# Performance work log

Measured on AMD Instinct MI355X. Metric: run time of the kernel, lower is better.

Reference implementation:

```python
import jax, jax.numpy as jnp
import numpy as np

N = 384          # residues / nodes
E = 12288        # edges (avg degree 32)
D_LM = 1024      # BERT hidden
D_NODE = 256     # extra node features -> D_LM + D_NODE = 1280
D = 1280         # node_emb_size
H = D // 10      # 128, dis/mask MLP hidden
M = 64           # masked positions


def setup_inputs() -> dict:
    key = jax.random.key(0)
    ks = jax.random.split(key, 16)
    s = lambda d_in: 1.0 / np.sqrt(d_in)
    inp = {
        "lm_embedding": jax.random.normal(ks[0], (1, N + 2, D_LM), jnp.float32),
        "node_feat": jax.random.normal(ks[1], (N, D_NODE), jnp.float32),
        # positive distances in [0.5, 1.5) so edge_weight = 1/(d^2+1e-6) is well scaled
        "edge_feat": jax.random.uniform(ks[2], (E, 1), jnp.float32) + 0.5,
        "src": jax.random.randint(ks[3], (E,), 0, N, jnp.int32),
        "dst": jax.random.randint(ks[4], (E,), 0, N, jnp.int32),
        "mask_index": jax.random.randint(ks[5], (M,), 0, N, jnp.int32),
        # GINConv apply-func linears (stored as [in, out]; torch Linear is x @ W.T + b)
        "W_gin0": jax.random.normal(ks[6], (D, D), jnp.float32) * s(D),
        "b_gin0": jnp.zeros((D,), jnp.float32),
        "W_gin1": jax.random.normal(ks[7], (D, D), jnp.float32) * s(D),
        "b_gin1": jnp.zeros((D,), jnp.float32),
        # dis_nn: Linear(D,H) -> ReLU -> Linear(H,30)
        "Wd1": jax.random.normal(ks[8], (D, H), jnp.float32) * s(D),
        "bd1": jnp.zeros((H,), jnp.float32),
        "Wd2": jax.random.normal(ks[9], (H, 30), jnp.float32) * s(H),
        "bd2": jnp.zeros((30,), jnp.float32),
        # mask_nn: Linear(D,H) -> ReLU -> Linear(H,2) -> Tanh
        "Wm1": jax.random.normal(ks[10], (D, H), jnp.float32) * s(D),
        "bm1": jnp.zeros((H,), jnp.float32),
        "Wm2": jax.random.normal(ks[11], (H, 2), jnp.float32) * s(H),
        "bm2": jnp.zeros((2,), jnp.float32),
    }
    return inp


def _gin(x, src, dst, edge_weight, W, b):
    # DGL GINConv (eps=0, 'sum'): Linear( x + sum_{e:(u->v)} w_e * x_u )
    msg = x[src] * edge_weight                      # [E, D] gather-multiply
    agg = jax.ops.segment_sum(msg, dst, num_segments=N)  # scatter-sum to dst
    return (x + agg) @ W + b


def reference(lm_embedding, node_feat, edge_feat, src, dst, mask_index,
              W_gin0, b_gin0, W_gin1, b_gin1,
              Wd1, bd1, Wd2, bd2, Wm1, bm1, Wm2, bm2):
    # node_feat0: strip CLS/SEP tokens, concat with node features -> [N, D]
    node_feat0 = jnp.concatenate([lm_embedding[0, 1:-1, :], node_feat], axis=1)
    edge_weight = 1.0 / (edge_feat ** 2 + 1e-6)     # [E, 1]

    # original uses node_feat0.data (detached) as GIN input
    x0 = jax.lax.stop_gradient(node_feat0)
    h = _gin(x0, src, dst, edge_weight, W_gin0, b_gin0)
    node_output = _gin(h, src, dst, edge_weight, W_gin1, b_gin1)
    node_output = node_output + node_feat0          # residual (use_lm=1)

    # pairwise squared differences: [N, N, D]
    dis_hid = (node_output[None, :, :] - node_output[:, None, :]) ** 2
    dh = dis_hid.reshape(-1, D)                     # [N*N, D]
    dis_pred = jax.nn.relu(dh @ Wd1 + bd1) @ Wd2 + bd2  # [N*N, 30]

    xm = node_output[mask_index]                    # [M, D]
    mask_pred = jnp.tanh(jax.nn.relu(xm @ Wm1 + bm1) @ Wm2 + bm2)  # [M, 2]
    return dis_pred, mask_pred
```

## Files before the change

kernel.cpp:

```cpp
#include <hip/hip_runtime.h>
#include <hip/hip_bf16.h>

#define NN 384
#define EE 12288
#define DD 1280
#define HH 128
#define DISROWS (NN*NN)

typedef short bf16x8 __attribute__((ext_vector_type(8)));
typedef short bf16x4 __attribute__((ext_vector_type(4)));
typedef float f32x4  __attribute__((ext_vector_type(4)));

__device__ __forceinline__ unsigned short f2bf(float x){
  unsigned u = __builtin_bit_cast(unsigned, x);
  u += 0x7fffu + ((u >> 16) & 1u);
  return (unsigned short)(u >> 16);
}
__device__ __forceinline__ float bf2f(unsigned short h){
  unsigned u = ((unsigned)h) << 16;
  return __builtin_bit_cast(float, u);
}
__device__ __forceinline__ short f2bf_fast(float x){
  return (short)__bfloat16_as_ushort(__float2bfloat16(x));
}
__device__ __forceinline__ void glds16(const short* g, short* l){
  __builtin_amdgcn_global_load_lds((const __attribute__((address_space(1))) void*)g,
                                   (__attribute__((address_space(3))) void*)l, 16, 0, 0);
}

__device__ __forceinline__ void tsplit_body(const float* __restrict__ W,
                                            short* __restrict__ Thi, short* __restrict__ Tlo,
                                            int R, int C, int bx, int by, int t,
                                            float* tile ){
  int rb = by*64, cb = bx*64;
  int r  = t >> 2;
  int cs = (t & 3) * 16;
  const float* sp = W + (long)(rb + r)*C + cb + cs;
  #pragma unroll
  for (int i = 0; i < 16; i += 4){
    f32x4 v = *(const f32x4*)(sp + i);
    tile[r*65 + cs+i+0] = v[0]; tile[r*65 + cs+i+1] = v[1];
    tile[r*65 + cs+i+2] = v[2]; tile[r*65 + cs+i+3] = v[3];
  }
  __syncthreads();
  int cp = t >> 2;
  int rs = (t & 3) * 16;
  bf16x8 vh0, vh1, vl0, vl1;
  #pragma unroll
  for (int i = 0; i < 8; ++i){
    float f = tile[(rs+i)*65 + cp];
    unsigned short h = f2bf(f);
    vh0[i] = (short)h; vl0[i] = (short)f2bf(f - bf2f(h));
  }
  #pragma unroll
  for (int i = 0; i < 8; ++i){
    float f = tile[(rs+8+i)*65 + cp];
    unsigned short h = f2bf(f);
    vh1[i] = (short)h; vl1[i] = (short)f2bf(f - bf2f(h));
  }
  long ob = (long)(cb + cp)*R + rb + rs;
  *(bf16x8*)&Thi[ob]   = vh0;
  *(bf16x8*)&Thi[ob+8] = vh1;
  if (Tlo){
    *(bf16x8*)&Tlo[ob]   = vl0;
    *(bf16x8*)&Tlo[ob+8] = vl1;
  }
}

__global__ void k_prep(const float* __restrict__ lm, const float* __restrict__ nf,
                       float* __restrict__ x0,
                       const int* __restrict__ dst, const float* __restrict__ ef,
                       int* __restrict__ offs, int* __restrict__ sorted,
                       float* __restrict__ ew,
                       const float* __restrict__ Wd1, short* __restrict__ W1t,
                       const float* __restrict__ Wd2, short* __restrict__ W2t,
                       const float* __restrict__ Wg0, short* __restrict__ WtAh,
                       short* __restrict__ WtAl){
  __shared__ __align__(16) float sh[64*65];
  const int b = blockIdx.x;
  const int t = threadIdx.x;
  if (b < 960){
    int i = b*512 + t;
    int n = i / 1280;
    int d = i - n*1280;
    x0[i] = (d < 1024) ? lm[(n+1)*1024 + d] : nf[n*256 + (d-1024)];
    return;
  }
  if (b == 960){
    int* cnt = (int*)sh;
    int* base = cnt + 512;
    if (t < 512) cnt[t] = 0;
    __syncthreads();
    for (int e = t; e < EE; e += 512){
      atomicAdd(&cnt[dst[e]], 1);
      float f = ef[e];
      ew[e] = 1.0f/(f*f + 1e-6f);
    }
    __syncthreads();
    for (int off = 1; off < 512; off <<= 1){
      int v = (t >= off) ? cnt[t - off] : 0;
      __syncthreads();
      cnt[t] += v;
      __syncthreads();
    }
    if (t < NN){
      int excl = t ? cnt[t-1] : 0;
      offs[t] = excl;
      base[t] = excl;
    }
    if (t == 0) offs[NN] = EE;
    __syncthreads();
    for (int e = t; e < EE; e += 512){
      int p = atomicAdd(&base[dst[e]], 1);
      sorted[p] = e;
    }
    return;
  }
  if (b < 1002){
    int g = b - 961;
    if (g < 40){
      if (t < 256) tsplit_body(Wd1, W1t, nullptr, DD, HH, g & 1, g >> 1, t, sh);
      else { __syncthreads(); }
      return;
    }
    for (int i = t; i < 32*HH; i += 512){
      int c = i >> 7, h = i & 127;
      float v = (c < 30) ? Wd2[h*30 + c] : 0.f;
      W2t[i] = (short)f2bf(v);
    }
    return;
  }
  {
    int g = b - 1002;
    if (t < 256) tsplit_body(Wg0, WtAh, WtAl, DD, DD, g % 20, g / 20, t, sh);
    else { __syncthreads(); }
  }
}

__global__ void k_agg(const float* __restrict__ X, const float* __restrict__ ew,
                      const int* __restrict__ src, const int* __restrict__ offs,
                      const int* __restrict__ sorted, float* __restrict__ Y){
  __shared__ int   s_off[160];
  __shared__ float s_w[160];
  const int v = blockIdx.x;
  const int d = blockIdx.y*256 + threadIdx.x;
  const int t = threadIdx.x;
  float acc = X[(long)v*DD + d];
  const int b = offs[v], e = offs[v+1];
  for (int c0 = b; c0 < e; c0 += 160){
    int n = e - c0; if (n > 160) n = 160;
    __syncthreads();
    if (t < n){
      int eid = sorted[c0 + t];
      s_off[t] = src[eid]*DD;
      s_w[t]   = ew[eid];
    }
    __syncthreads();
    int k = 0;
    for (; k + 4 <= n; k += 4){
      acc += s_w[k]  *X[s_off[k]   + d];
      acc += s_w[k+1]*X[s_off[k+1] + d];
      acc += s_w[k+2]*X[s_off[k+2] + d];
      acc += s_w[k+3]*X[s_off[k+3] + d];
    }
    for (; k < n; ++k) acc += s_w[k]*X[s_off[k] + d];
  }
  Y[(long)v*DD + d] = acc;
}

__launch_bounds__(256, 2)
__global__ void k_gin_gemm(const float* __restrict__ Y, const short* __restrict__ Whi,
                           const short* __restrict__ Wlo, float* __restrict__ P){
  __shared__ __align__(16) short Ahi[128*40], Alo[128*40], Bhi[128*40], Blo[128*40];
  const int m0 = blockIdx.x*128;
  const int n0 = blockIdx.y*128;
  const int kbase = blockIdx.z*320;
  const int t = threadIdx.x, w = t >> 6, lane = t & 63;
  const int l15 = lane & 15, l4 = lane >> 4;
  f32x4 acc[2][8];
  #pragma unroll
  for (int m = 0; m < 2; ++m)
    #pragma unroll
    for (int n = 0; n < 8; ++n) acc[m][n] = (f32x4){0.f,0.f,0.f,0.f};

  const int row = t >> 1, half = t & 1;
  const float* ap  = Y   + (long)(m0+row)*DD + half*16;
  const short* bph = Whi + (long)(n0+row)*DD + half*16;
  const short* bpl = Wlo + (long)(n0+row)*DD + half*16;

  for (int kk = 0; kk < 10; ++kk){
    int d0 = kbase + kk*32;
    __syncthreads();
    #pragma unroll
    for (int g = 0; g < 2; ++g){
      f32x4 v0 = *(const f32x4*)(ap + d0 + g*8);
      f32x4 v1 = *(const f32x4*)(ap + d0 + g*8 + 4);
      bf16x8 vh, vl;
      #pragma unroll
      for (int q = 0; q < 4; ++q){
        unsigned short h0 = f2bf(v0[q]);
        vh[q]   = (short)h0; vl[q]   = (short)f2bf(v0[q] - bf2f(h0));
        unsigned short h1 = f2bf(v1[q]);
        vh[4+q] = (short)h1; vl[4+q] = (short)f2bf(v1[q] - bf2f(h1));
      }
      *(bf16x8*)&Ahi[row*40 + half*16 + g*8] = vh;
      *(bf16x8*)&Alo[row*40 + half*16 + g*8] = vl;
    }
    *(bf16x8*)&Bhi[row*40 + half*16]     = *(const bf16x8*)(bph + d0);
    *(bf16x8*)&Bhi[row*40 + half*16 + 8] = *(const bf16x8*)(bph + d0 + 8);
    *(bf16x8*)&Blo[row*40 + half*16]     = *(const bf16x8*)(bpl + d0);
    *(bf16x8*)&Blo[row*40 + half*16 + 8] = *(const bf16x8*)(bpl + d0 + 8);
    __syncthreads();

    bf16x8 ah[2], al[2];
    #pragma unroll
    for (int m = 0; m < 2; ++m){
      int rr = w*32 + m*16 + l15;
      ah[m] = *(const bf16x8*)&Ahi[rr*40 + l4*8];
      al[m] = *(const bf16x8*)&Alo[rr*40 + l4*8];
    }
    #pragma unroll
    for (int n = 0; n < 8; ++n){
      int rr = n*16 + l15;
      bf16x8 bh = *(const bf16x8*)&Bhi[rr*40 + l4*8];
      bf16x8 bl = *(const bf16x8*)&Blo[rr*40 + l4*8];
      #pragma unroll
      for (int m = 0; m < 2; ++m){
        acc[m][n] = __builtin_amdgcn_mfma_f32_16x16x32_bf16(ah[m], bh, acc[m][n], 0,0,0);
        acc[m][n] = __builtin_amdgcn_mfma_f32_16x16x32_bf16(ah[m], bl, acc[m][n], 0,0,0);
        acc[m][n] = __builtin_amdgcn_mfma_f32_16x16x32_bf16(al[m], bh, acc[m][n], 0,0,0);
      }
    }
  }
  float* Pz = P + (long)blockIdx.z*NN*DD;
  #pragma unroll
  for (int m = 0; m < 2; ++m){
    #pragma unroll
    for (int n = 0; n < 8; ++n){
      int gr0 = m0 + w*32 + m*16 + l4*4;
      int gc  = n0 + n*16 + l15;
      #pragma unroll
      for (int r = 0; r < 4; ++r)
        Pz[(long)(gr0+r)*DD + gc] = acc[m][n][r];
    }
  }
}

__global__ void k_red_t(const float* __restrict__ P, const float* __restrict__ bias,
                        const float* __restrict__ resid, float* __restrict__ Out,
                        const float* __restrict__ Wg1, short* __restrict__ WtAh,
                        short* __restrict__ WtAl){
  __shared__ __align__(16) float sh[64*65];
  const int b = blockIdx.x;
  if (b >= 480){
    if (Wg1){
      int g = b - 480;
      tsplit_body(Wg1, WtAh, WtAl, DD, DD, g % 20, g / 20, threadIdx.x, sh);
    }
    return;
  }
  const int i = b*256 + threadIdx.x;
  const int col = (i*4) % DD;
  const f32x4* P4 = (const f32x4*)P;
  f32x4 s = P4[i];
  s += P4[i + 122880];
  s += P4[i + 2*122880];
  s += P4[i + 3*122880];
  s += *(const f32x4*)(bias + col);
  if (resid) s += ((const f32x4*)resid)[i];
  ((f32x4*)Out)[i] = s;
}

__launch_bounds__(256, 3)
__global__ void k_dis(const float* __restrict__ X, const short* __restrict__ W1t,
                      const float* __restrict__ bd1, const short* __restrict__ W2t,
                      const float* __restrict__ bd2, float* __restrict__ out,
                      const int* __restrict__ midx,
                      const float* __restrict__ Wm1, const float* __restrict__ bm1,
                      const float* __restrict__ Wm2, const float* __restrict__ bm2){
  __shared__ __align__(16) short smem[25088];
  const int b = blockIdx.x;
  const int t = threadIdx.x;

  if (b >= 600){
    float* tl = (float*)smem;
    int m = b - 600;
    if (t < HH){
      const float* x = X + (long)midx[m]*DD;
      float a0 = 0.f, a1 = 0.f, a2 = 0.f, a3 = 0.f;
      for (int d = 0; d < DD; d += 4){
        a0 += x[d]   * Wm1[(d)*HH + t];
        a1 += x[d+1] * Wm1[(d+1)*HH + t];
        a2 += x[d+2] * Wm1[(d+2)*HH + t];
        a3 += x[d+3] * Wm1[(d+3)*HH + t];
      }
      float v = a0 + a1 + a2 + a3 + bm1[t];
      tl[t] = v > 0.f ? v : 0.f;
    }
    __syncthreads();
    if (t < 2){
      float s = bm2[t];
      for (int h = 0; h < HH; ++h) s += tl[h]*Wm2[h*2 + t];
      out[(long)DISROWS*30 + m*2 + t] = tanhf(s);
    }
    return;
  }

  int k = 0, rem = b;
  while (rem >= 2*(24 - k)){ rem -= 2*(24 - k); ++k; }
  int ib = 2*k;
  if (rem >= 24 - k){ ++ib; rem -= 24 - k; }
  const int jb = k + rem;
  const int i0 = ib*8, j0 = jb*16;

  const int w = t >> 6, lane = t & 63;
  const int l15 = lane & 15, l4 = lane >> 4;

  short* WA = smem;
  float* XF = (float*)(smem + 16384);
  short* TL = smem;
  float* OT = (float*)(smem + 17408);

  f32x4 acc[2][8];
  #pragma unroll
  for (int m = 0; m < 2; ++m)
    #pragma unroll
    for (int n = 0; n < 8; ++n) acc[m][n] = (f32x4){0.f,0.f,0.f,0.f};

  const short* wsrc[4];
  #pragma unroll
  for (int i = 0; i < 4; ++i){
    int hb = w*32 + i*8 + (lane >> 3);
    wsrc[i] = W1t + (long)hb*DD + (((lane & 7) ^ (hb & 7))*8);
  }
  const float* xsrc[6];
  int xli[6];
  #pragma unroll
  for (int g = 0; g < 6; ++g){
    int idx = g*256 + t;
    int rowl = idx >> 6, col = idx & 63;
    int grow = (rowl < 8) ? (i0 + rowl) : (j0 + rowl - 8);
    xsrc[g] = X + (long)grow*DD + col;
    xli[g] = rowl*68 + col;
  }

  float xr[6];
  #pragma unroll
  for (int i = 0; i < 4; ++i)
    glds16(wsrc[i], WA + (w*32 + i*8)*64);
  #pragma unroll
  for (int g = 0; g < 6; ++g) xr[g] = xsrc[g][0];
  #pragma unroll
  for (int g = 0; g < 6; ++g) XF[xli[g]] = xr[g];
  __syncthreads();

  for (int mk = 0; mk < 20; ++mk){
    const int cb = mk & 1;
    short* WAc = WA + cb*8192;
    float* XFc = XF + cb*1632;
    short* WAn = WA + (cb^1)*8192;
    float* XFn = XF + (cb^1)*1632;
    if (mk < 19){
      #pragma unroll
      for (int i = 0; i < 4; ++i)
        glds16(wsrc[i] + (mk+1)*64, WAn + (w*32 + i*8)*64);
      #pragma unroll
      for (int g = 0; g < 6; ++g) xr[g] = xsrc[g][(mk+1)*64];
    }
    #pragma unroll
    for (int ks = 0; ks < 2; ++ks){
      f32x4 xj0 = *(const f32x4*)&XFc[(8 + l15)*68 + ks*32 + l4*8];
      f32x4 xj1 = *(const f32x4*)&XFc[(8 + l15)*68 + ks*32 + l4*8 + 4];
      bf16x8 a[2];
      #pragma unroll
      for (int m = 0; m < 2; ++m){
        const float* xip = &XFc[(2*w + m)*68 + ks*32 + l4*8];
        f32x4 xi0 = *(const f32x4*)xip;
        f32x4 xi1 = *(const f32x4*)(xip + 4);
        bf16x8 av;
        #pragma unroll
        for (int q = 0; q < 4; ++q){ float dl = xj0[q]-xi0[q]; av[q]   = f2bf_fast(dl*dl); }
        #pragma unroll
        for (int q = 0; q < 4; ++q){ float dl = xj1[q]-xi1[q]; av[4+q] = f2bf_fast(dl*dl); }
        a[m] = av;
      }
      #pragma unroll
      for (int n = 0; n < 8; ++n){
        bf16x8 wf = *(const bf16x8*)&WAc[(n*16 + l15)*64 + (((ks*4 + l4) ^ (l15 & 7))*8)];
        acc[0][n] = __builtin_amdgcn_mfma_f32_16x16x32_bf16(wf, a[0], acc[0][n], 0,0,0);
        acc[1][n] = __builtin_amdgcn_mfma_f32_16x16x32_bf16(wf, a[1], acc[1][n], 0,0,0);
      }
    }
    if (mk < 19){
      #pragma unroll
      for (int g = 0; g < 6; ++g) XFn[xli[g]] = xr[g];
    }
    __syncthreads();
  }

  f32x4 bd1v[8];
  #pragma unroll
  for (int n = 0; n < 8; ++n) bd1v[n] = *(const f32x4*)(bd1 + n*16 + l4*4);
  #pragma unroll
  for (int m = 0; m < 2; ++m){
    int pair = (2*w + m)*16 + l15;
    #pragma unroll
    for (int n = 0; n < 8; ++n){
      bf16x4 pv;
      #pragma unroll
      for (int r = 0; r < 4; ++r){
        float v = acc[m][n][r] + bd1v[n][r];
        v = v > 0.f ? v : 0.f;
        pv[r] = f2bf_fast(v);
      }
      *(bf16x4*)&TL[pair*136 + n*16 + l4*4] = pv;
    }
  }
  __syncthreads();

  f32x4 acc2[2][2];
  #pragma unroll
  for (int m2 = 0; m2 < 2; ++m2)
    #pragma unroll
    for (int nn = 0; nn < 2; ++nn) acc2[m2][nn] = (f32x4){0.f,0.f,0.f,0.f};
  #pragma unroll
  for (int hs = 0; hs < 4; ++hs){
    bf16x8 b2[2];
    #pragma unroll
    for (int nn = 0; nn < 2; ++nn)
      b2[nn] = *(const bf16x8*)&W2t[(nn*16 + l15)*HH + hs*32 + l4*8];
    #pragma unroll
    for (int m2 = 0; m2 < 2; ++m2){
      bf16x8 a2 = *(const bf16x8*)&TL[(w*32 + m2*16 + l15)*136 + hs*32 + l4*8];
      #pragma unroll
      for (int nn = 0; nn < 2; ++nn)
        acc2[m2][nn] = __builtin_amdgcn_mfma_f32_16x16x32_bf16(a2, b2[nn], acc2[m2][nn], 0,0,0);
    }
  }
  #pragma unroll
  for (int m2 = 0; m2 < 2; ++m2){
    #pragma unroll
    for (int nn = 0; nn < 2; ++nn){
      int cc = nn*16 + l15;
      if (cc < 30){
        float b2v = bd2[cc];
        #pragma unroll
        for (int r = 0; r < 4; ++r)
          OT[(w*32 + m2*16 + l4*4 + r)*30 + cc] = acc2[m2][nn][r] + b2v;
      }
    }
  }
  __syncthreads();

  {
    int i = t >> 5;
    int ca = (t & 31)*15;
    long nbase = ((long)(i0 + i)*NN + j0)*30 + ca;
    const float* nsrc = OT + i*480 + ca;
    #pragma unroll
    for (int q = 0; q < 15; ++q) out[nbase + q] = nsrc[q];
    int j = t >> 4;
    int s = t & 15;
    int ii = s >> 1;
    int c0 = (s & 1)*15;
    long mbase = ((long)(j0 + j)*NN + i0 + ii)*30 + c0;
    const float* msrc = OT + ii*480 + j*30 + c0;
    #pragma unroll
    for (int q = 0; q < 15; ++q) out[mbase + q] = msrc[q];
  }
}

extern "C" void kernel_launch(void* const* d_in, const int* in_sizes, int n_in,
                              void* d_out, int out_size, void* d_ws, size_t ws_size,
                              hipStream_t stream){
  const float* lm   = (const float*)d_in[0];
  const float* nf   = (const float*)d_in[1];
  const float* ef   = (const float*)d_in[2];
  const int*   src  = (const int*)d_in[3];
  const int*   dst  = (const int*)d_in[4];
  const int*   midx = (const int*)d_in[5];
  const float* Wg0  = (const float*)d_in[6];
  const float* bg0  = (const float*)d_in[7];
  const float* Wg1  = (const float*)d_in[8];
  const float* bg1  = (const float*)d_in[9];
  const float* Wd1  = (const float*)d_in[10];
  const float* bd1  = (const float*)d_in[11];
  const float* Wd2  = (const float*)d_in[12];
  const float* bd2  = (const float*)d_in[13];
  const float* Wm1  = (const float*)d_in[14];
  const float* bm1  = (const float*)d_in[15];
  const float* Wm2  = (const float*)d_in[16];
  const float* bm2  = (const float*)d_in[17];
  float* dis = (float*)d_out;

  char* ws = (char*)d_ws;
  size_t off = 0;
  auto alloc = [&](size_t bytes)->void*{
    void* p = ws + off; off += (bytes + 255) & ~(size_t)255; return p;
  };
  float* x0   = (float*)alloc((size_t)NN*DD*4);
  float* yb   = (float*)alloc((size_t)NN*DD*4);
  float* hb   = (float*)alloc((size_t)NN*DD*4);
  float* ew   = (float*)alloc((size_t)EE*4);
  int*   offs = (int*)alloc((NN+1)*4);
  int*   sorted = (int*)alloc(EE*4);
  short* WtAh = (short*)alloc((size_t)DD*DD*2);
  short* WtAl = (short*)alloc((size_t)DD*DD*2);
  short* W1t  = (short*)alloc((size_t)HH*DD*2);
  short* W2t  = (short*)alloc((size_t)32*HH*2);
  float* P    = (float*)alloc((size_t)4*NN*DD*4);

  k_prep<<<1402,512,0,stream>>>(lm, nf, x0, dst, ef, offs, sorted, ew,
                                Wd1, W1t, Wd2, W2t, Wg0, WtAh, WtAl);

  k_agg<<<dim3(384,5),256,0,stream>>>(x0, ew, src, offs, sorted, yb);
  k_gin_gemm<<<dim3(3,10,4),256,0,stream>>>(yb, WtAh, WtAl, P);
  k_red_t<<<880,256,0,stream>>>(P, bg0, nullptr, hb, Wg1, WtAh, WtAl);

  k_agg<<<dim3(384,5),256,0,stream>>>(hb, ew, src, offs, sorted, yb);
  k_gin_gemm<<<dim3(3,10,4),256,0,stream>>>(yb, WtAh, WtAl, P);
  k_red_t<<<480,256,0,stream>>>(P, bg1, x0, hb, nullptr, nullptr, nullptr);

  k_dis<<<664,256,0,stream>>>(hb, W1t, bd1, W2t, bd2, dis,
                              midx, Wm1, bm1, Wm2, bm2);
}
```

Before: 142.3 us.

## Drop split-K GIN GEMM, fuse epilogue, and enlarge dis tiles to 16x16

The GIN GEMM moves from a 128x128 split-K tile plus a separate reduction kernel to a 64x64 full-K tile. Bias and residual are now applied in the epilogue, which removes the partial-sum buffer and the reduce kernel. Both GIN weight transposes move into the prep kernel, using separate buffers. The pairwise distance kernel now uses 16x16 i/j tiles (half as many blocks) with a 32-wide K step, a new swizzle, and a two-pass second-layer/store phase, so each W1 slice loaded is reused across more pairs. In exchange, the GIN GEMM has fewer blocks doing longer K loops, the prep kernel grows, and the dis kernel uses more registers per thread.

Result: slower. 197.5 us (+38.8%).

```diff
diff --git a/kernel.cpp b/kernel.cpp
--- a/kernel.cpp
+++ b/kernel.cpp
@@ -10,6 +10,7 @@
 typedef short bf16x8 __attribute__((ext_vector_type(8)));
 typedef short bf16x4 __attribute__((ext_vector_type(4)));
 typedef float f32x4  __attribute__((ext_vector_type(4)));
+typedef float f32x2  __attribute__((ext_vector_type(2)));
 
 __device__ __forceinline__ unsigned short f2bf(float x){
   unsigned u = __builtin_bit_cast(unsigned, x);
@@ -75,7 +76,9 @@
                        const float* __restrict__ Wd1, short* __restrict__ W1t,
                        const float* __restrict__ Wd2, short* __restrict__ W2t,
                        const float* __restrict__ Wg0, short* __restrict__ WtAh,
-                       short* __restrict__ WtAl){
+                       short* __restrict__ WtAl,
+                       const float* __restrict__ Wg1, short* __restrict__ WtBh,
+                       short* __restrict__ WtBl){
   __shared__ __align__(16) float sh[64*65];
   const int b = blockIdx.x;
   const int t = threadIdx.x;
@@ -130,9 +133,15 @@
     }
     return;
   }
-  {
+  if (b < 1402){
     int g = b - 1002;
     if (t < 256) tsplit_body(Wg0, WtAh, WtAl, DD, DD, g % 20, g / 20, t, sh);
+    else { __syncthreads(); }
+    return;
+  }
+  {
+    int g = b - 1402;
+    if (t < 256) tsplit_body(Wg1, WtBh, WtBl, DD, DD, g % 20, g / 20, t, sh);
     else { __syncthreads(); }
   }
 }
@@ -169,109 +178,67 @@
 }
 
 __launch_bounds__(256, 2)
-__global__ void k_gin_gemm(const float* __restrict__ Y, const short* __restrict__ Whi,
-                           const short* __restrict__ Wlo, float* __restrict__ P){
-  __shared__ __align__(16) short Ahi[128*40], Alo[128*40], Bhi[128*40], Blo[128*40];
-  const int m0 = blockIdx.x*128;
-  const int n0 = blockIdx.y*128;
-  const int kbase = blockIdx.z*320;
+__global__ void k_gin(const float* __restrict__ Y, const short* __restrict__ Whi,
+                      const short* __restrict__ Wlo, const float* __restrict__ bias,
+                      const float* __restrict__ resid, float* __restrict__ Out){
+  __shared__ __align__(16) short Ahi[64*40], Alo[64*40], Bhi[64*40], Blo[64*40];
+  const int m0 = blockIdx.x*64, n0 = blockIdx.y*64;
   const int t = threadIdx.x, w = t >> 6, lane = t & 63;
   const int l15 = lane & 15, l4 = lane >> 4;
-  f32x4 acc[2][8];
-  #pragma unroll
-  for (int m = 0; m < 2; ++m)
-    #pragma unroll
-    for (int n = 0; n < 8; ++n) acc[m][n] = (f32x4){0.f,0.f,0.f,0.f};
-
-  const int row = t >> 1, half = t & 1;
-  const float* ap  = Y   + (long)(m0+row)*DD + half*16;
-  const short* bph = Whi + (long)(n0+row)*DD + half*16;
-  const short* bpl = Wlo + (long)(n0+row)*DD + half*16;
-
-  for (int kk = 0; kk < 10; ++kk){
-    int d0 = kbase + kk*32;
-    __syncthreads();
-    #pragma unroll
-    for (int g = 0; g < 2; ++g){
-      f32x4 v0 = *(const f32x4*)(ap + d0 + g*8);
-      f32x4 v1 = *(const f32x4*)(ap + d0 + g*8 + 4);
-      bf16x8 vh, vl;
-      #pragma unroll
-      for (int q = 0; q < 4; ++q){
-        unsigned short h0 = f2bf(v0[q]);
-        vh[q]   = (short)h0; vl[q]   = (short)f2bf(v0[q] - bf2f(h0));
-        unsigned short h1 = f2bf(v1[q]);
-        vh[4+q] = (short)h1; vl[4+q] = (short)f2bf(v1[q] - bf2f(h1));
-      }
-      *(bf16x8*)&Ahi[row*40 + half*16 + g*8] = vh;
-      *(bf16x8*)&Alo[row*40 + half*16 + g*8] = vl;
-    }
-    *(bf16x8*)&Bhi[row*40 + half*16]     = *(const bf16x8*)(bph + d0);
-    *(bf16x8*)&Bhi[row*40 + half*16 + 8] = *(const bf16x8*)(bph + d0 + 8);
-    *(bf16x8*)&Blo[row*40 + half*16]     = *(const bf16x8*)(bpl + d0);
-    *(bf16x8*)&Blo[row*40 + half*16 + 8] = *(const bf16x8*)(bpl + d0 + 8);
-    __syncthreads();
-
-    bf16x8 ah[2], al[2];
-    #pragma unroll
-    for (int m = 0; m < 2; ++m){
-      int rr = w*32 + m*16 + l15;
-      ah[m] = *(const bf16x8*)&Ahi[rr*40 + l4*8];
-      al[m] = *(const bf16x8*)&Alo[rr*40 + l4*8];
-    }
-    #pragma unroll
-    for (int n = 0; n < 8; ++n){
-      int rr = n*16 + l15;
-      bf16x8 bh = *(const bf16x8*)&Bhi[rr*40 + l4*8];
-      bf16x8 bl = *(const bf16x8*)&Blo[rr*40 + l4*8];
-      #pragma unroll
-      for (int m = 0; m < 2; ++m){
-        acc[m][n] = __builtin_amdgcn_mfma_f32_16x16x32_bf16(ah[m], bh, acc[m][n], 0,0,0);
-        acc[m][n] = __builtin_amdgcn_mfma_f32_16x16x32_bf16(ah[m], bl, acc[m][n], 0,0,0);
-        acc[m][n] = __builtin_amdgcn_mfma_f32_16x16x32_bf16(al[m], bh, acc[m][n], 0,0,0);
-      }
-    }
-  }
-  float* Pz = P + (long)blockIdx.z*NN*DD;
-  #pragma unroll
-  for (int m = 0; m < 2; ++m){
-    #pragma unroll
-    for (int n = 0; n < 8; ++n){
-      int gr0 = m0 + w*32 + m*16 + l4*4;
-      int gc  = n0 + n*16 + l15;
-      #pragma unroll
-      for (int r = 0; r < 4; ++r)
-        Pz[(long)(gr0+r)*DD + gc] = acc[m][n][r];
-    }
-  }
-}
-
-__global__ void k_red_t(const float* __restrict__ P, const float* __restrict__ bias,
-                        const float* __restrict__ resid, float* __restrict__ Out,
-                        const float* __restrict__ Wg1, short* __restrict__ WtAh,
-                        short* __restrict__ WtAl){
-  __shared__ __align__(16) float sh[64*65];
-  const int b = blockIdx.x;
-  if (b >= 480){
-    if (Wg1){
-      int g = b - 480;
-      tsplit_body(Wg1, WtAh, WtAl, DD, DD, g % 20, g / 20, threadIdx.x, sh);
-    }
-    return;
-  }
-  const int i = b*256 + threadIdx.x;
-  const int col = (i*4) % DD;
-  const f32x4* P4 = (const f32x4*)P;
-  f32x4 s = P4[i];
-  s += P4[i + 122880];
-  s += P4[i + 2*122880];
-  s += P4[i + 3*122880];
-  s += *(const f32x4*)(bias + col);
-  if (resid) s += ((const f32x4*)resid)[i];
-  ((f32x4*)Out)[i] = s;
-}
-
-__launch_bounds__(256, 3)
+  f32x4 acc[4];
+  #pragma unroll
+  for (int n = 0; n < 4; ++n) acc[n] = (f32x4){0.f,0.f,0.f,0.f};
+
+  const int row = t >> 2, q = t & 3;
+  const float* ap  = Y   + (long)(m0+row)*DD + q*8;
+  const short* bph = Whi + (long)(n0+row)*DD + q*8;
+  const short* bpl = Wlo + (long)(n0+row)*DD + q*8;
+
+  for (int kk = 0; kk < 40; ++kk){
+    const int d0 = kk*32;
+    __syncthreads();
+    f32x4 v0 = *(const f32x4*)(ap + d0);
+    f32x4 v1 = *(const f32x4*)(ap + d0 + 4);
+    bf16x8 vh, vl;
+    #pragma unroll
+    for (int qq = 0; qq < 4; ++qq){
+      unsigned short h0 = f2bf(v0[qq]);
+      vh[qq]   = (short)h0; vl[qq]   = (short)f2bf(v0[qq] - bf2f(h0));
+      unsigned short h1 = f2bf(v1[qq]);
+      vh[4+qq] = (short)h1; vl[4+qq] = (short)f2bf(v1[qq] - bf2f(h1));
+    }
+    *(bf16x8*)&Ahi[row*40 + q*8] = vh;
+    *(bf16x8*)&Alo[row*40 + q*8] = vl;
+    *(bf16x8*)&Bhi[row*40 + q*8] = *(const bf16x8*)(bph + d0);
+    *(bf16x8*)&Blo[row*40 + q*8] = *(const bf16x8*)(bpl + d0);
+    __syncthreads();
+
+    bf16x8 ah = *(const bf16x8*)&Ahi[(w*16 + l15)*40 + l4*8];
+    bf16x8 al = *(const bf16x8*)&Alo[(w*16 + l15)*40 + l4*8];
+    #pragma unroll
+    for (int n = 0; n < 4; ++n){
+      bf16x8 bh = *(const bf16x8*)&Bhi[(n*16 + l15)*40 + l4*8];
+      bf16x8 bl = *(const bf16x8*)&Blo[(n*16 + l15)*40 + l4*8];
+      acc[n] = __builtin_amdgcn_mfma_f32_16x16x32_bf16(ah, bh, acc[n], 0,0,0);
+      acc[n] = __builtin_amdgcn_mfma_f32_16x16x32_bf16(ah, bl, acc[n], 0,0,0);
+      acc[n] = __builtin_amdgcn_mfma_f32_16x16x32_bf16(al, bh, acc[n], 0,0,0);
+    }
+  }
+  #pragma unroll
+  for (int n = 0; n < 4; ++n){
+    int gc = n0 + n*16 + l15;
+    float bv = bias[gc];
+    #pragma unroll
+    for (int r = 0; r < 4; ++r){
+      int gr = m0 + w*16 + l4*4 + r;
+      float o = acc[n][r] + bv;
+      if (resid) o += resid[(long)gr*DD + gc];
+      Out[(long)gr*DD + gc] = o;
+    }
+  }
+}
+
+__launch_bounds__(256, 2)
 __global__ void k_dis(const float* __restrict__ X, const short* __restrict__ W1t,
                       const float* __restrict__ bd1, const short* __restrict__ W2t,
                       const float* __restrict__ bd2, float* __restrict__ out,
@@ -282,9 +249,9 @@
   const int b = blockIdx.x;
   const int t = threadIdx.x;
 
-  if (b >= 600){
+  if (b >= 300){
     float* tl = (float*)smem;
-    int m = b - 600;
+    int m = b - 300;
     if (t < HH){
       const float* x = X + (long)midx[m]*DD;
       float a0 = 0.f, a1 = 0.f, a2 = 0.f, a3 = 0.f;
@@ -306,167 +273,171 @@
     return;
   }
 
-  int k = 0, rem = b;
-  while (rem >= 2*(24 - k)){ rem -= 2*(24 - k); ++k; }
-  int ib = 2*k;
-  if (rem >= 24 - k){ ++ib; rem -= 24 - k; }
-  const int jb = k + rem;
-  const int i0 = ib*8, j0 = jb*16;
+  int ib = 0, rem = b;
+  while (rem >= 24 - ib){ rem -= 24 - ib; ++ib; }
+  const int jb = ib + rem;
+  const int i0 = ib*16, j0 = jb*16;
 
   const int w = t >> 6, lane = t & 63;
   const int l15 = lane & 15, l4 = lane >> 4;
 
   short* WA = smem;
-  float* XF = (float*)(smem + 16384);
+  float* XJ = (float*)(smem + 8192);
   short* TL = smem;
   float* OT = (float*)(smem + 17408);
 
-  f32x4 acc[2][8];
-  #pragma unroll
-  for (int m = 0; m < 2; ++m)
+  f32x4 acc[4][8];
+  #pragma unroll
+  for (int m = 0; m < 4; ++m)
     #pragma unroll
     for (int n = 0; n < 8; ++n) acc[m][n] = (f32x4){0.f,0.f,0.f,0.f};
 
-  const short* wsrc[4];
-  #pragma unroll
-  for (int i = 0; i < 4; ++i){
-    int hb = w*32 + i*8 + (lane >> 3);
-    wsrc[i] = W1t + (long)hb*DD + (((lane & 7) ^ (hb & 7))*8);
-  }
-  const float* xsrc[6];
-  int xli[6];
-  #pragma unroll
-  for (int g = 0; g < 6; ++g){
-    int idx = g*256 + t;
-    int rowl = idx >> 6, col = idx & 63;
-    int grow = (rowl < 8) ? (i0 + rowl) : (j0 + rowl - 8);
-    xsrc[g] = X + (long)grow*DD + col;
-    xli[g] = rowl*68 + col;
-  }
-
-  float xr[6];
-  #pragma unroll
-  for (int i = 0; i < 4; ++i)
-    glds16(wsrc[i], WA + (w*32 + i*8)*64);
-  #pragma unroll
-  for (int g = 0; g < 6; ++g) xr[g] = xsrc[g][0];
-  #pragma unroll
-  for (int g = 0; g < 6; ++g) XF[xli[g]] = xr[g];
+  const short* wsrc[2]; int wdst[2];
+  #pragma unroll
+  for (int i = 0; i < 2; ++i){
+    int h = (w*2 + i)*16 + (lane >> 2);
+    int s = lane & 3;
+    wsrc[i] = W1t + (long)h*DD + ((s ^ ((h >> 1) & 3))*8);
+    wdst[i] = (w*2 + i)*512;
+  }
+  const float* xjsrc = X + (long)(j0 + (t >> 4))*DD + (t & 15)*2;
+  const int xjli = (t >> 4)*36 + (t & 15)*2;
+  const float* xip[4];
+  #pragma unroll
+  for (int m = 0; m < 4; ++m)
+    xip[m] = X + (long)(i0 + w*4 + m)*DD + l4*8;
+
+  glds16(wsrc[0], WA + wdst[0]);
+  glds16(wsrc[1], WA + wdst[1]);
+  { f32x2 v = *(const f32x2*)xjsrc; *(f32x2*)&XJ[xjli] = v; }
+  f32x4 xa[4], xb[4];
+  #pragma unroll
+  for (int m = 0; m < 4; ++m){
+    xa[m] = *(const f32x4*)xip[m];
+    xb[m] = *(const f32x4*)(xip[m] + 4);
+  }
   __syncthreads();
 
-  for (int mk = 0; mk < 20; ++mk){
-    const int cb = mk & 1;
-    short* WAc = WA + cb*8192;
-    float* XFc = XF + cb*1632;
-    short* WAn = WA + (cb^1)*8192;
-    float* XFn = XF + (cb^1)*1632;
-    if (mk < 19){
-      #pragma unroll
-      for (int i = 0; i < 4; ++i)
-        glds16(wsrc[i] + (mk+1)*64, WAn + (w*32 + i*8)*64);
-      #pragma unroll
-      for (int g = 0; g < 6; ++g) xr[g] = xsrc[g][(mk+1)*64];
-    }
-    #pragma unroll
-    for (int ks = 0; ks < 2; ++ks){
-      f32x4 xj0 = *(const f32x4*)&XFc[(8 + l15)*68 + ks*32 + l4*8];
-      f32x4 xj1 = *(const f32x4*)&XFc[(8 + l15)*68 + ks*32 + l4*8 + 4];
-      bf16x8 a[2];
-      #pragma unroll
-      for (int m = 0; m < 2; ++m){
-        const float* xip = &XFc[(2*w + m)*68 + ks*32 + l4*8];
-        f32x4 xi0 = *(const f32x4*)xip;
-        f32x4 xi1 = *(const f32x4*)(xip + 4);
-        bf16x8 av;
+  const int wro = (l4 ^ ((l15 >> 1) & 3))*8;
+  for (int mk = 0; mk < 40; ++mk){
+    const int cur = mk & 1, nxt = cur ^ 1;
+    f32x2 xjn; f32x4 xan[4], xbn[4];
+    if (mk < 39){
+      const int d1 = (mk+1)*32;
+      glds16(wsrc[0] + d1, WA + nxt*4096 + wdst[0]);
+      glds16(wsrc[1] + d1, WA + nxt*4096 + wdst[1]);
+      xjn = *(const f32x2*)(xjsrc + d1);
+      #pragma unroll
+      for (int m = 0; m < 4; ++m){
+        xan[m] = *(const f32x4*)(xip[m] + d1);
+        xbn[m] = *(const f32x4*)(xip[m] + d1 + 4);
+      }
+    }
+    const float* XJc = XJ + cur*576;
+    f32x4 xj0 = *(const f32x4*)&XJc[l15*36 + l4*8];
+    f32x4 xj1 = *(const f32x4*)&XJc[l15*36 + l4*8 + 4];
+    bf16x8 a[4];
+    #pragma unroll
+    for (int m = 0; m < 4; ++m){
+      bf16x8 av;
+      #pragma unroll
+      for (int q = 0; q < 4; ++q){ float d = xj0[q]-xa[m][q]; av[q]   = f2bf_fast(d*d); }
+      #pragma unroll
+      for (int q = 0; q < 4; ++q){ float d = xj1[q]-xb[m][q]; av[4+q] = f2bf_fast(d*d); }
+      a[m] = av;
+    }
+    const short* WAc = WA + cur*4096;
+    #pragma unroll
+    for (int n = 0; n < 8; ++n){
+      bf16x8 wf = *(const bf16x8*)&WAc[(n*16 + l15)*32 + wro];
+      #pragma unroll
+      for (int m = 0; m < 4; ++m)
+        acc[m][n] = __builtin_amdgcn_mfma_f32_16x16x32_bf16(wf, a[m], acc[m][n], 0,0,0);
+    }
+    if (mk < 39){
+      *(f32x2*)&XJ[nxt*576 + xjli] = xjn;
+      #pragma unroll
+      for (int m = 0; m < 4; ++m){ xa[m] = xan[m]; xb[m] = xbn[m]; }
+    }
+    __syncthreads();
+  }
+
+  f32x4 bd1v[8];
+  #pragma unroll
+  for (int n = 0; n < 8; ++n) bd1v[n] = *(const f32x4*)(bd1 + n*16 + l4*4);
+
+  for (int c = 0; c < 2; ++c){
+    if ((w >> 1) == c){
+      #pragma unroll
+      for (int m = 0; m < 4; ++m){
+        int pair = ((w & 1)*4 + m)*16 + l15;
         #pragma unroll
-        for (int q = 0; q < 4; ++q){ float dl = xj0[q]-xi0[q]; av[q]   = f2bf_fast(dl*dl); }
+        for (int n = 0; n < 8; ++n){
+          bf16x4 pv;
+          #pragma unroll
+          for (int r = 0; r < 4; ++r){
+            float v = acc[m][n][r] + bd1v[n][r];
+            v = v > 0.f ? v : 0.f;
+            pv[r] = f2bf_fast(v);
+          }
+          *(bf16x4*)&TL[pair*136 + n*16 + l4*4] = pv;
+        }
+      }
+    }
+    __syncthreads();
+
+    f32x4 acc2[2][2];
+    #pragma unroll
+    for (int m2 = 0; m2 < 2; ++m2)
+      #pragma unroll
+      for (int nn = 0; nn < 2; ++nn) acc2[m2][nn] = (f32x4){0.f,0.f,0.f,0.f};
+    #pragma unroll
+    for (int hs = 0; hs < 4; ++hs){
+      bf16x8 b2[2];
+      #pragma unroll
+      for (int nn = 0; nn < 2; ++nn)
+        b2[nn] = *(const bf16x8*)&W2t[(nn*16 + l15)*HH + hs*32 + l4*8];
+      #pragma unroll
+      for (int m2 = 0; m2 < 2; ++m2){
+        bf16x8 a2 = *(const bf16x8*)&TL[(w*32 + m2*16 + l15)*136 + hs*32 + l4*8];
         #pragma unroll
-        for (int q = 0; q < 4; ++q){ float dl = xj1[q]-xi1[q]; av[4+q] = f2bf_fast(dl*dl); }
-        a[m] = av;
+        for (int nn = 0; nn < 2; ++nn)
+          acc2[m2][nn] = __builtin_amdgcn_mfma_f32_16x16x32_bf16(a2, b2[nn], acc2[m2][nn], 0,0,0);
       }
-      #pragma unroll
-      for (int n = 0; n < 8; ++n){
-        bf16x8 wf = *(const bf16x8*)&WAc[(n*16 + l15)*64 + (((ks*4 + l4) ^ (l15 & 7))*8)];
-        acc[0][n] = __builtin_amdgcn_mfma_f32_16x16x32_bf16(wf, a[0], acc[0][n], 0,0,0);
-        acc[1][n] = __builtin_amdgcn_mfma_f32_16x16x32_bf16(wf, a[1], acc[1][n], 0,0,0);
+    }
+    #pragma unroll
+    for (int m2 = 0; m2 < 2; ++m2){
+      #pragma unroll
+      for (int nn = 0; nn < 2; ++nn){
+        int cc = nn*16 + l15;
+        if (cc < 30){
+          float b2v = bd2[cc];
+          #pragma unroll
+          for (int r = 0; r < 4; ++r)
+            OT[(w*32 + m2*16 + l4*4 + r)*30 + cc] = acc2[m2][nn][r] + b2v;
+        }
       }
     }
-    if (mk < 19){
-      #pragma unroll
-      for (int g = 0; g < 6; ++g) XFn[xli[g]] = xr[g];
-    }
-    __syncthreads();
-  }
-
-  f32x4 bd1v[8];
-  #pragma unroll
-  for (int n = 0; n < 8; ++n) bd1v[n] = *(const f32x4*)(bd1 + n*16 + l4*4);
-  #pragma unroll
-  for (int m = 0; m < 2; ++m){
-    int pair = (2*w + m)*16 + l15;
-    #pragma unroll
-    for (int n = 0; n < 8; ++n){
-      bf16x4 pv;
-      #pragma unroll
-      for (int r = 0; r < 4; ++r){
-        float v = acc[m][n][r] + bd1v[n][r];
-        v = v > 0.f ? v : 0.f;
-        pv[r] = f2bf_fast(v);
-      }
-      *(bf16x4*)&TL[pair*136 + n*16 + l4*4] = pv;
-    }
-  }
-  __syncthreads();
-
-  f32x4 acc2[2][2];
-  #pragma unroll
-  for (int m2 = 0; m2 < 2; ++m2)
-    #pragma unroll
-    for (int nn = 0; nn < 2; ++nn) acc2[m2][nn] = (f32x4){0.f,0.f,0.f,0.f};
-  #pragma unroll
-  for (int hs = 0; hs < 4; ++hs){
-    bf16x8 b2[2];
-    #pragma unroll
-    for (int nn = 0; nn < 2; ++nn)
-      b2[nn] = *(const bf16x8*)&W2t[(nn*16 + l15)*HH + hs*32 + l4*8];
-    #pragma unroll
-    for (int m2 = 0; m2 < 2; ++m2){
-      bf16x8 a2 = *(const bf16x8*)&TL[(w*32 + m2*16 + l15)*136 + hs*32 + l4*8];
-      #pragma unroll
-      for (int nn = 0; nn < 2; ++nn)
-        acc2[m2][nn] = __builtin_amdgcn_mfma_f32_16x16x32_bf16(a2, b2[nn], acc2[m2][nn], 0,0,0);
-    }
-  }
-  #pragma unroll
-  for (int m2 = 0; m2 < 2; ++m2){
-    #pragma unroll
-    for (int nn = 0; nn < 2; ++nn){
-      int cc = nn*16 + l15;
-      if (cc < 30){
-        float b2v = bd2[cc];
-        #pragma unroll
-        for (int r = 0; r < 4; ++r)
-          OT[(w*32 + m2*16 + l4*4 + r)*30 + cc] = acc2[m2][nn][r] + b2v;
-      }
-    }
-  }
-  __syncthreads();
-
-  {
-    int i = t >> 5;
-    int ca = (t & 31)*15;
-    long nbase = ((long)(i0 + i)*NN + j0)*30 + ca;
-    const float* nsrc = OT + i*480 + ca;
-    #pragma unroll
-    for (int q = 0; q < 15; ++q) out[nbase + q] = nsrc[q];
-    int j = t >> 4;
-    int s = t & 15;
-    int ii = s >> 1;
-    int c0 = (s & 1)*15;
-    long mbase = ((long)(j0 + j)*NN + i0 + ii)*30 + c0;
-    const float* msrc = OT + ii*480 + j*30 + c0;
-    #pragma unroll
-    for (int q = 0; q < 15; ++q) out[mbase + q] = msrc[q];
+    __syncthreads();
+
+    {
+      const int i0c = i0 + c*8;
+      int i = t >> 5;
+      int ca = (t & 31)*15;
+      long nbase = ((long)(i0c + i)*NN + j0)*30 + ca;
+      const float* nsrc = OT + i*480 + ca;
+      #pragma unroll
+      for (int q = 0; q < 15; ++q) out[nbase + q] = nsrc[q];
+      int j = t >> 4;
+      int s = t & 15;
+      int ii = s >> 1;
+      int c0 = (s & 1)*15;
+      long mbase = ((long)(j0 + j)*NN + i0c + ii)*30 + c0;
+      const float* msrc = OT + ii*480 + j*30 + c0;
+      #pragma unroll
+      for (int q = 0; q < 15; ++q) out[mbase + q] = msrc[q];
+    }
+    if (c == 0) __syncthreads();
   }
 }
 
@@ -506,21 +477,21 @@
   int*   sorted = (int*)alloc(EE*4);
   short* WtAh = (short*)alloc((size_t)DD*DD*2);
   short* WtAl = (short*)alloc((size_t)DD*DD*2);
+  short* WtBh = (short*)alloc((size_t)DD*DD*2);
+  short* WtBl = (short*)alloc((size_t)DD*DD*2);
   short* W1t  = (short*)alloc((size_t)HH*DD*2);
   short* W2t  = (short*)alloc((size_t)32*HH*2);
-  float* P    = (float*)alloc((size_t)4*NN*DD*4);
-
-  k_prep<<<1402,512,0,stream>>>(lm, nf, x0, dst, ef, offs, sorted, ew,
-                                Wd1, W1t, Wd2, W2t, Wg0, WtAh, WtAl);
+
+  k_prep<<<1802,512,0,stream>>>(lm, nf, x0, dst, ef, offs, sorted, ew,
+                                Wd1, W1t, Wd2, W2t,
+                                Wg0, WtAh, WtAl, Wg1, WtBh, WtBl);
 
   k_agg<<<dim3(384,5),256,0,stream>>>(x0, ew, src, offs, sorted, yb);
-  k_gin_gemm<<<dim3(3,10,4),256,0,stream>>>(yb, WtAh, WtAl, P);
-  k_red_t<<<880,256,0,stream>>>(P, bg0, nullptr, hb, Wg1, WtAh, WtAl);
+  k_gin<<<dim3(6,20),256,0,stream>>>(yb, WtAh, WtAl, bg0, nullptr, hb);
 
   k_agg<<<dim3(384,5),256,0,stream>>>(hb, ew, src, offs, sorted, yb);
-  k_gin_gemm<<<dim3(3,10,4),256,0,stream>>>(yb, WtAh, WtAl, P);
-  k_red_t<<<480,256,0,stream>>>(P, bg1, x0, hb, nullptr, nullptr, nullptr);
-
-  k_dis<<<664,256,0,stream>>>(hb, W1t, bd1, W2t, bd2, dis,
+  k_gin<<<dim3(6,20),256,0,stream>>>(yb, WtBh, WtBl, bg1, x0, hb);
+
+  k_dis<<<364,256,0,stream>>>(hb, W1t, bd1, W2t, bd2, dis,
                               midx, Wm1, bm1, Wm2, bm2);
 }
```
